# Optimization experiments

Measured on AMD Instinct MI355X. Metric: run time of the kernel, lower is better.

The kernel has to match this reference:

```python
import jax, jax.numpy as jnp
import numpy as np

N_NODES = 100000
N_EDGES = 1600000
D_IN = 128
D_OUT = 128


def setup_inputs() -> dict:
    key = jax.random.key(0)
    ks = jax.random.split(key, 8)
    x = jax.random.normal(ks[0], (N_NODES, D_IN), dtype=jnp.float32)
    edge_index = jax.random.randint(ks[1], (2, N_EDGES), 0, N_NODES, dtype=jnp.int64)
    s1 = 1.0 / np.sqrt(D_IN)
    s2 = 1.0 / np.sqrt(D_OUT)
    # SAGEConv: lin_l acts on aggregated neighbors (has bias), lin_r on self (no bias)
    Wl1 = jax.random.uniform(ks[2], (D_OUT, D_IN), jnp.float32, -s1, s1)
    Wr1 = jax.random.uniform(ks[3], (D_OUT, D_IN), jnp.float32, -s1, s1)
    b1 = jnp.zeros((D_OUT,), jnp.float32)
    Wl2 = jax.random.uniform(ks[4], (D_OUT, D_OUT), jnp.float32, -s2, s2)
    Wr2 = jax.random.uniform(ks[5], (D_OUT, D_OUT), jnp.float32, -s2, s2)
    b2 = jnp.zeros((D_OUT,), jnp.float32)
    return {"x": x, "edge_index": edge_index, "Wl1": Wl1, "Wr1": Wr1, "b1": b1,
            "Wl2": Wl2, "Wr2": Wr2, "b2": b2}


def _sage_conv(x, src, dst, Wl, Wr, b, n_nodes):
    # mean aggregation of source features at destination nodes
    agg = jax.ops.segment_sum(x[src], dst, num_segments=n_nodes)  # [N, d]
    deg = jax.ops.segment_sum(jnp.ones((src.shape[0],), x.dtype), dst, num_segments=n_nodes)
    mean = agg / jnp.maximum(deg, 1.0)[:, None]  # isolated nodes -> 0 (PyG scatter-mean)
    return mean @ Wl.T + b + x @ Wr.T


def reference(x, edge_index, Wl1, Wr1, b1, Wl2, Wr2, b2):
    src, dst = edge_index[0], edge_index[1]
    n = x.shape[0]
    h = _sage_conv(x, src, dst, Wl1, Wr1, b1, n)
    h = _sage_conv(h, src, dst, Wl2, Wr2, b2, n)
    return h
```

## Files before the change

### kernel.cpp

```cpp
#include <hip/hip_runtime.h>
#include <hip/hip_bf16.h>

#define D 128
#define SCAN_CHUNK 1024
#define TE 4096

typedef __attribute__((ext_vector_type(8))) short bf16x8;
typedef __attribute__((ext_vector_type(4))) float f32x4;
typedef __attribute__((ext_vector_type(2))) float f32x2;

__device__ __forceinline__ bool ei_is64(const int* ei32) {
    return (ei32[1] | ei32[3] | ei32[5] | ei32[7]) == 0;
}
__device__ __forceinline__ int get_idx(const void* ei, bool is64, long long pos) {
    return is64 ? (int)((const long long*)ei)[pos] : ((const int*)ei)[pos];
}

__global__ __launch_bounds__(256) void prep_kernel(
    const float* __restrict__ x, unsigned* __restrict__ xq, long long ND, int ncvt,
    const float* __restrict__ Wl1, const float* __restrict__ Wr1,
    const float* __restrict__ Wl2, const float* __restrict__ Wr2,
    ushort* __restrict__ Wf1, ushort* __restrict__ Wf2,
    const void* __restrict__ ei, int E, int NB, int NBLK, int SH,
    int* __restrict__ histT) {
    __shared__ int h[512];
    const int t = threadIdx.x;
    int bid = blockIdx.x;

    if (bid < ncvt) {
        long long i = ((long long)bid * 256 + t) * 8;
        if (i + 7 < ND) {
            float4 v0 = *reinterpret_cast<const float4*>(x + i);
            float4 v1 = *reinterpret_cast<const float4*>(x + i + 4);
            int p0 = __builtin_amdgcn_cvt_pk_fp8_f32(v0.x, v0.y, 0, false);
            p0 = __builtin_amdgcn_cvt_pk_fp8_f32(v0.z, v0.w, p0, true);
            int p1 = __builtin_amdgcn_cvt_pk_fp8_f32(v1.x, v1.y, 0, false);
            p1 = __builtin_amdgcn_cvt_pk_fp8_f32(v1.z, v1.w, p1, true);
            *reinterpret_cast<uint2*>(reinterpret_cast<unsigned char*>(xq) + i) =
                make_uint2((unsigned)p0, (unsigned)p1);
        } else {
            for (; i < ND; ++i) {
                int pk = __builtin_amdgcn_cvt_pk_fp8_f32(x[i], x[i], 0, false);
                reinterpret_cast<unsigned char*>(xq)[i] = (unsigned char)(pk & 0xff);
            }
        }
        return;
    }
    bid -= ncvt;
    if (bid < 32) {
        int gid = bid * 256 + t;
        int id = gid & 4095;
        const float* Wl = Wl1; const float* Wr = Wr1; ushort* Wf = Wf1;
        if (gid >= 4096) { Wl = Wl2; Wr = Wr2; Wf = Wf2; }
        int lane = id & 63, s = (id >> 6) & 7, j = id >> 9;
        int c = j * 16 + (lane & 15);
        int k = s * 32 + ((lane >> 4) << 3);
        const float* src = (k < 128) ? (Wl + c * 128 + k) : (Wr + c * 128 + (k - 128));
        float4 v0 = *reinterpret_cast<const float4*>(src);
        float4 v1 = *reinterpret_cast<const float4*>(src + 4);
        __hip_bfloat16 o[8];
        o[0] = __float2bfloat16(v0.x); o[1] = __float2bfloat16(v0.y);
        o[2] = __float2bfloat16(v0.z); o[3] = __float2bfloat16(v0.w);
        o[4] = __float2bfloat16(v1.x); o[5] = __float2bfloat16(v1.y);
        o[6] = __float2bfloat16(v1.z); o[7] = __float2bfloat16(v1.w);
        *reinterpret_cast<uint4*>(Wf + (size_t)id * 8) = *reinterpret_cast<uint4*>(o);
        return;
    }
    bid -= 32;
    for (int b = t; b < 512; b += 256) h[b] = 0;
    bool is64 = ei_is64((const int*)ei);
    __syncthreads();
    const int base = bid * TE;
    for (int i = t; i < TE; i += 256) {
        int e = base + i;
        if (e < E) {
            int d = get_idx(ei, is64, (long long)E + e);
            atomicAdd(&h[d >> SH], 1);
        }
    }
    __syncthreads();
    for (int b = t; b < NB; b += 256) histT[b * NBLK + bid] = h[b];
}

__global__ __launch_bounds__(256) void scan_partial_kernel(int* __restrict__ arr, int Ntot,
                                                           int* __restrict__ bsum) {
    __shared__ int ws[256];
    const int t = threadIdx.x;
    const int i0 = blockIdx.x * SCAN_CHUNK + t * 4;
    int4 v = {0, 0, 0, 0};
    if (i0 + 3 < Ntot) {
        v = *reinterpret_cast<const int4*>(arr + i0);
    } else {
        if (i0 < Ntot) v.x = arr[i0];
        if (i0 + 1 < Ntot) v.y = arr[i0 + 1];
        if (i0 + 2 < Ntot) v.z = arr[i0 + 2];
        if (i0 + 3 < Ntot) v.w = arr[i0 + 3];
    }
    ws[t] = v.x + v.y + v.z + v.w;
    __syncthreads();
    for (int off = 1; off < 256; off <<= 1) {
        int val = (t >= off) ? ws[t - off] : 0;
        __syncthreads();
        ws[t] += val;
        __syncthreads();
    }
    int ex = t ? ws[t - 1] : 0;
    int e0 = ex, e1 = ex + v.x, e2 = e1 + v.y, e3 = e2 + v.z;
    if (i0 + 3 < Ntot) {
        *reinterpret_cast<int4*>(arr + i0) = make_int4(e0, e1, e2, e3);
    } else {
        if (i0 < Ntot) arr[i0] = e0;
        if (i0 + 1 < Ntot) arr[i0 + 1] = e1;
        if (i0 + 2 < Ntot) arr[i0 + 2] = e2;
        if (i0 + 3 < Ntot) arr[i0 + 3] = e3;
    }
    if (t == 255) bsum[blockIdx.x] = ws[255];
}

__device__ __forceinline__ void scan_bsum_lds(const int* __restrict__ bsum, int nb2,
                                              int* sb) {
    const int t = threadIdx.x;
    sb[t] = (t < nb2) ? bsum[t] : 0;
    __syncthreads();
    for (int off = 1; off < 256; off <<= 1) {
        int v = (t >= off) ? sb[t - off] : 0;
        __syncthreads();
        sb[t] += v;
        __syncthreads();
    }
}

__global__ __launch_bounds__(256) void part_scatter_kernel(const void* __restrict__ ei, int E,
                                                           int NB, int NBLK, int SH,
                                                           const int* __restrict__ histT,
                                                           const int* __restrict__ bsum,
                                                           int nb2,
                                                           unsigned* __restrict__ ebuf) {
    __shared__ int cur[512];
    __shared__ int sb[256];
    const int t = threadIdx.x;
    bool is64 = ei_is64((const int*)ei);
    scan_bsum_lds(bsum, nb2, sb);
    for (int b = t; b < NB; b += 256) {
        int idx = b * NBLK + blockIdx.x;
        int c = idx >> 10;
        cur[b] = histT[idx] + (c ? sb[c - 1] : 0);
    }
    __syncthreads();
    const int base = blockIdx.x * TE;
    for (int i = t; i < TE; i += 256) {
        int e = base + i;
        if (e < E) {
            int s = get_idx(ei, is64, e);
            int d = get_idx(ei, is64, (long long)E + e);
            int pos = atomicAdd(&cur[d >> SH], 1);
            ebuf[pos] = (unsigned)s | ((unsigned)(d & ((1 << SH) - 1)) << 24);
        }
    }
}

__global__ __launch_bounds__(256) void bucket_csr_kernel(const unsigned* __restrict__ ebuf,
                                                         const int* __restrict__ histT,
                                                         const int* __restrict__ bsum,
                                                         int nb2,
                                                         int NB, int NBLK, int SH, int E,
                                                         int N, int* __restrict__ rs,
                                                         int* __restrict__ col) {
    const int b = blockIdx.x, t = threadIdx.x;
    const int nodes = 1 << SH;
    __shared__ int h[256];
    __shared__ int cur[256];
    __shared__ int sb[256];
    __shared__ int sse[2];
    scan_bsum_lds(bsum, nb2, sb);
    if (t == 0) {
        int i0 = b * NBLK;
        int c0 = i0 >> 10;
        sse[0] = histT[i0] + (c0 ? sb[c0 - 1] : 0);
        if (b + 1 < NB) {
            int i1 = (b + 1) * NBLK;
            int c1 = i1 >> 10;
            sse[1] = histT[i1] + (c1 ? sb[c1 - 1] : 0);
        } else {
            sse[1] = E;
        }
    }
    h[t] = 0;
    __syncthreads();
    const int bstart = sse[0], bend = sse[1];
    for (int i = bstart + t; i < bend; i += 256) {
        atomicAdd(&h[ebuf[i] >> 24], 1);
    }
    __syncthreads();
    for (int off = 1; off < nodes; off <<= 1) {
        int v = (t >= off) ? h[t - off] : 0;
        __syncthreads();
        h[t] += v;
        __syncthreads();
    }
    const int node0 = b << SH;
    {
        int node = node0 + t;
        if (node < N) rs[node] = bstart + h[t];
        cur[t] = bstart + (t ? h[t - 1] : 0);
    }
    __syncthreads();
    for (int i = bstart + t; i < bend; i += 256) {
        unsigned ed = ebuf[i];
        int pos = atomicAdd(&cur[ed >> 24], 1);
        col[pos] = (int)(ed & 0xFFFFFFu);
    }
}

__device__ __forceinline__ void acc8(f32x2& a0, f32x2& a1, f32x2& a2, f32x2& a3,
                                     uint2 d) {
    a0 += __builtin_amdgcn_cvt_pk_f32_fp8((int)d.x, false);
    a1 += __builtin_amdgcn_cvt_pk_f32_fp8((int)d.x, true);
    a2 += __builtin_amdgcn_cvt_pk_f32_fp8((int)d.y, false);
    a3 += __builtin_amdgcn_cvt_pk_f32_fp8((int)d.y, true);
}

__global__ __launch_bounds__(256) void aggregate_mean_fp8_kernel(
    const unsigned char* __restrict__ xq, const int* __restrict__ rs,
    const int* __restrict__ col, ushort* __restrict__ outm, int N) {
    const int t = threadIdx.x;
    const int v = blockIdx.x * 16 + (t >> 4);
    if (v >= N) return;
    const unsigned lcoff = (unsigned)(t & 15) * 8u;
    const int start = v ? rs[v - 1] : 0, end = rs[v];
    f32x2 a0 = {0.f, 0.f}, a1 = {0.f, 0.f}, a2 = {0.f, 0.f}, a3 = {0.f, 0.f};
    int e = start;
    for (; e + 7 < end; e += 8) {
        int c0 = col[e], c1 = col[e + 1], c2 = col[e + 2], c3 = col[e + 3];
        int c4 = col[e + 4], c5 = col[e + 5], c6 = col[e + 6], c7 = col[e + 7];
        uint2 d0 = *reinterpret_cast<const uint2*>(xq + (((unsigned)c0) << 7) + lcoff);
        uint2 d1 = *reinterpret_cast<const uint2*>(xq + (((unsigned)c1) << 7) + lcoff);
        uint2 d2 = *reinterpret_cast<const uint2*>(xq + (((unsigned)c2) << 7) + lcoff);
        uint2 d3 = *reinterpret_cast<const uint2*>(xq + (((unsigned)c3) << 7) + lcoff);
        uint2 d4 = *reinterpret_cast<const uint2*>(xq + (((unsigned)c4) << 7) + lcoff);
        uint2 d5 = *reinterpret_cast<const uint2*>(xq + (((unsigned)c5) << 7) + lcoff);
        uint2 d6 = *reinterpret_cast<const uint2*>(xq + (((unsigned)c6) << 7) + lcoff);
        uint2 d7 = *reinterpret_cast<const uint2*>(xq + (((unsigned)c7) << 7) + lcoff);
        acc8(a0, a1, a2, a3, d0); acc8(a0, a1, a2, a3, d1);
        acc8(a0, a1, a2, a3, d2); acc8(a0, a1, a2, a3, d3);
        acc8(a0, a1, a2, a3, d4); acc8(a0, a1, a2, a3, d5);
        acc8(a0, a1, a2, a3, d6); acc8(a0, a1, a2, a3, d7);
    }
    for (; e + 3 < end; e += 4) {
        int c0 = col[e], c1 = col[e + 1], c2 = col[e + 2], c3 = col[e + 3];
        uint2 d0 = *reinterpret_cast<const uint2*>(xq + (((unsigned)c0) << 7) + lcoff);
        uint2 d1 = *reinterpret_cast<const uint2*>(xq + (((unsigned)c1) << 7) + lcoff);
        uint2 d2 = *reinterpret_cast<const uint2*>(xq + (((unsigned)c2) << 7) + lcoff);
        uint2 d3 = *reinterpret_cast<const uint2*>(xq + (((unsigned)c3) << 7) + lcoff);
        acc8(a0, a1, a2, a3, d0); acc8(a0, a1, a2, a3, d1);
        acc8(a0, a1, a2, a3, d2); acc8(a0, a1, a2, a3, d3);
    }
    if (e < end) {
        const int l = end - 1;
        int i1 = e + 1 < end ? e + 1 : l;
        int i2 = e + 2 < end ? e + 2 : l;
        int c0 = col[e], c1 = col[i1], c2 = col[i2];
        uint2 d0 = *reinterpret_cast<const uint2*>(xq + (((unsigned)c0) << 7) + lcoff);
        uint2 d1 = *reinterpret_cast<const uint2*>(xq + (((unsigned)c1) << 7) + lcoff);
        uint2 d2 = *reinterpret_cast<const uint2*>(xq + (((unsigned)c2) << 7) + lcoff);
        d1.x = (e + 1 < end) ? d1.x : 0u; d1.y = (e + 1 < end) ? d1.y : 0u;
        d2.x = (e + 2 < end) ? d2.x : 0u; d2.y = (e + 2 < end) ? d2.y : 0u;
        acc8(a0, a1, a2, a3, d0); acc8(a0, a1, a2, a3, d1);
        acc8(a0, a1, a2, a3, d2);
    }
    float inv = (end > start) ? 1.0f / (float)(end - start) : 0.f;
    __hip_bfloat16 o[8];
    o[0] = __float2bfloat16(a0.x * inv); o[1] = __float2bfloat16(a0.y * inv);
    o[2] = __float2bfloat16(a1.x * inv); o[3] = __float2bfloat16(a1.y * inv);
    o[4] = __float2bfloat16(a2.x * inv); o[5] = __float2bfloat16(a2.y * inv);
    o[6] = __float2bfloat16(a3.x * inv); o[7] = __float2bfloat16(a3.y * inv);
    *reinterpret_cast<uint4*>(outm + (size_t)v * D + ((t & 15) << 3)) =
        *reinterpret_cast<uint4*>(o);
}

template <typename OutT, bool DUAL, bool SELFF32>
__global__ __launch_bounds__(512) void sage_mfma_kernel(
    const ushort* __restrict__ Ab, const void* __restrict__ Sb,
    const ushort* __restrict__ Wf, const float* __restrict__ bias,
    OutT* __restrict__ out, unsigned char* __restrict__ fq, int N) {
    __shared__ uint4 ldsB[4096];
    const int t = threadIdx.x;
    {
        const uint4* g = reinterpret_cast<const uint4*>(Wf);
#pragma unroll
        for (int i = 0; i < 8; ++i) ldsB[t + i * 512] = g[t + i * 512];
    }
    __syncthreads();

    const int lane = t & 63, w = t >> 6;
    const int lm = lane & 15;
    const int ksub = (lane >> 4) * 8;
    const int mbase = blockIdx.x * 128 + w * 16;

    int r0 = mbase + lm;
    if (r0 >= N) r0 = N - 1;

    f32x4 acc[8];
#pragma unroll
    for (int j = 0; j < 8; ++j) {
        float bv = bias[j * 16 + lm];
        acc[j] = {bv, bv, bv, bv};
    }

    const ushort* A0 = Ab + (size_t)r0 * D + ksub;
    const ushort* lB = reinterpret_cast<const ushort*>(ldsB) + lane * 8;

#pragma unroll
    for (int s = 0; s < 8; ++s) {
        bf16x8 a;
        if (s < 4) {
            a = *reinterpret_cast<const bf16x8*>(A0 + s * 32);
        } else if constexpr (SELFF32) {
            const float* S0 = (const float*)Sb + (size_t)r0 * D + (s - 4) * 32 + ksub;
            float4 v0 = *reinterpret_cast<const float4*>(S0);
            float4 v1 = *reinterpret_cast<const float4*>(S0 + 4);
            __hip_bfloat16 o[8];
            o[0] = __float2bfloat16(v0.x); o[1] = __float2bfloat16(v0.y);
            o[2] = __float2bfloat16(v0.z); o[3] = __float2bfloat16(v0.w);
            o[4] = __float2bfloat16(v1.x); o[5] = __float2bfloat16(v1.y);
            o[6] = __float2bfloat16(v1.z); o[7] = __float2bfloat16(v1.w);
            a = *reinterpret_cast<bf16x8*>(o);
        } else {
            const ushort* S0 = (const ushort*)Sb + (size_t)r0 * D + ksub;
            a = *reinterpret_cast<const bf16x8*>(S0 + (s - 4) * 32);
        }
#pragma unroll
        for (int j = 0; j < 8; ++j) {
            bf16x8 b = *reinterpret_cast<const bf16x8*>(lB + (j * 8 + s) * 512);
            acc[j] = __builtin_amdgcn_mfma_f32_16x16x32_bf16(a, b, acc[j], 0, 0, 0);
        }
    }

    const int rr = (lane >> 4) * 4;
#pragma unroll
    for (int r = 0; r < 4; ++r) {
        int row = mbase + rr + r;
        if (row < N) {
#pragma unroll
            for (int j = 0; j < 8; ++j) {
                float val = acc[j][r];
                if constexpr (sizeof(OutT) == 2)
                    out[(size_t)row * D + j * 16 + lm] = __float2bfloat16(val);
                else
                    out[(size_t)row * D + j * 16 + lm] = val;
                if constexpr (DUAL) {
                    int pk = __builtin_amdgcn_cvt_pk_fp8_f32(val, val, 0, false);
                    fq[(size_t)row * D + j * 16 + lm] = (unsigned char)(pk & 0xff);
                }
            }
        }
    }
}

extern "C" void kernel_launch(void* const* d_in, const int* in_sizes, int n_in,
                              void* d_out, int out_size, void* d_ws, size_t ws_size,
                              hipStream_t stream) {
    const float* x   = (const float*)d_in[0];
    const void*  ei  = d_in[1];
    const float* Wl1 = (const float*)d_in[2];
    const float* Wr1 = (const float*)d_in[3];
    const float* b1  = (const float*)d_in[4];
    const float* Wl2 = (const float*)d_in[5];
    const float* Wr2 = (const float*)d_in[6];
    const float* b2  = (const float*)d_in[7];
    float* out = (float*)d_out;

    const int N = in_sizes[0] / D;
    const int E = in_sizes[1] / 2;
    const long long ND = (long long)N * D;

    int SH = 8;
    while (((N + (1 << SH) - 1) >> SH) > 512) ++SH;
    const int NB = (N + (1 << SH) - 1) >> SH;
    const int NBLK = (E + TE - 1) / TE;
    const int Ntot = NB * NBLK;
    const int nb2 = (Ntot + SCAN_CHUNK - 1) / SCAN_CHUNK;

    ushort* meanb = (ushort*)d_ws;
    ushort* h1b   = meanb + ND;
    ushort* Wf1   = h1b + ND;
    ushort* Wf2   = Wf1 + 32768;
    int*    rs    = (int*)(Wf2 + 32768);
    int*    col   = rs + N;
    int*      histT = (int*)meanb;
    int*      bsum  = histT + Ntot;
    unsigned* ebuf  = (unsigned*)h1b;
    unsigned char* xq  = (unsigned char*)d_out;
    unsigned char* h1q = (unsigned char*)d_out + ND;

    const int ncvt = (int)((ND / 8 + 255) / 256);

    prep_kernel<<<ncvt + 32 + NBLK, 256, 0, stream>>>(
        x, (unsigned*)xq, ND, ncvt, Wl1, Wr1, Wl2, Wr2,
        Wf1, Wf2, ei, E, NB, NBLK, SH, histT);

    scan_partial_kernel<<<nb2, 256, 0, stream>>>(histT, Ntot, bsum);
    part_scatter_kernel<<<NBLK, 256, 0, stream>>>(ei, E, NB, NBLK, SH, histT, bsum, nb2, ebuf);
    bucket_csr_kernel<<<NB, 256, 0, stream>>>(ebuf, histT, bsum, nb2, NB, NBLK, SH, E, N, rs, col);

    const int agg_grid = (N + 15) / 16;
    const int gemm_grid = (N + 127) / 128;

    aggregate_mean_fp8_kernel<<<agg_grid, 256, 0, stream>>>(xq, rs, col, meanb, N);
    sage_mfma_kernel<__hip_bfloat16, true, true><<<gemm_grid, 512, 0, stream>>>(
        meanb, x, Wf1, b1, (__hip_bfloat16*)h1b, h1q, N);

    aggregate_mean_fp8_kernel<<<agg_grid, 256, 0, stream>>>(h1q, rs, col, meanb, N);
    sage_mfma_kernel<float, false, false><<<gemm_grid, 512, 0, stream>>>(
        meanb, h1b, Wf2, b2, out, nullptr, N);
}
```

Baseline: 160.9 us.

## Sort nodes by degree within aggregation blocks to balance wavefront work

The aggregation kernel now handles 32 nodes per 512-thread block. It loads each node's CSR range into shared memory and ranks the nodes by degree, so each 64-lane wavefront processes four nodes of similar degree. This is meant to cut divergence from degree imbalance inside a wavefront. The 4-edge remainder loop is replaced by one masked 7-wide tail. The cost is two block barriers, a small rank computation per block, and redundant masked loads in the tail.

```diff
diff --git a/kernel.cpp b/kernel.cpp
--- a/kernel.cpp
+++ b/kernel.cpp
@@ -220,14 +220,36 @@
     a3 += __builtin_amdgcn_cvt_pk_f32_fp8((int)d.y, true);
 }
 
-__global__ __launch_bounds__(256) void aggregate_mean_fp8_kernel(
+__global__ __launch_bounds__(512) void aggregate_mean_fp8_kernel(
     const unsigned char* __restrict__ xq, const int* __restrict__ rs,
     const int* __restrict__ col, ushort* __restrict__ outm, int N) {
-    const int t = threadIdx.x;
-    const int v = blockIdx.x * 16 + (t >> 4);
-    if (v >= N) return;
+    __shared__ int s_start[32], s_end[32], s_map[32];
+    const int t = threadIdx.x;
+    if (t < 32) {
+        int v = blockIdx.x * 32 + t;
+        int st = 0, en = 0;
+        if (v < N) { st = v ? rs[v - 1] : 0; en = rs[v]; }
+        s_start[t] = st; s_end[t] = en;
+    }
+    __syncthreads();
+    if (t < 32) {
+        int d = s_end[t] - s_start[t];
+        int r = 0;
+#pragma unroll
+        for (int j = 0; j < 32; ++j) {
+            int dj = s_end[j] - s_start[j];
+            r += (dj < d) || (dj == d && j < t);
+        }
+        s_map[r] = t;
+    }
+    __syncthreads();
+
+    const int Q = t >> 4;
+    const int li = s_map[Q];
+    const int v = blockIdx.x * 32 + li;
+    const int start = s_start[li], end = s_end[li];
     const unsigned lcoff = (unsigned)(t & 15) * 8u;
-    const int start = v ? rs[v - 1] : 0, end = rs[v];
+
     f32x2 a0 = {0.f, 0.f}, a1 = {0.f, 0.f}, a2 = {0.f, 0.f}, a3 = {0.f, 0.f};
     int e = start;
     for (; e + 7 < end; e += 8) {
@@ -246,36 +268,44 @@
         acc8(a0, a1, a2, a3, d4); acc8(a0, a1, a2, a3, d5);
         acc8(a0, a1, a2, a3, d6); acc8(a0, a1, a2, a3, d7);
     }
-    for (; e + 3 < end; e += 4) {
-        int c0 = col[e], c1 = col[e + 1], c2 = col[e + 2], c3 = col[e + 3];
+    if (e < end) {
+        const int l = end - 1;
+        int i1 = e + 1 < end ? e + 1 : l;
+        int i2 = e + 2 < end ? e + 2 : l;
+        int i3 = e + 3 < end ? e + 3 : l;
+        int i4 = e + 4 < end ? e + 4 : l;
+        int i5 = e + 5 < end ? e + 5 : l;
+        int i6 = e + 6 < end ? e + 6 : l;
+        int c0 = col[e], c1 = col[i1], c2 = col[i2], c3 = col[i3];
+        int c4 = col[i4], c5 = col[i5], c6 = col[i6];
         uint2 d0 = *reinterpret_cast<const uint2*>(xq + (((unsigned)c0) << 7) + lcoff);
         uint2 d1 = *reinterpret_cast<const uint2*>(xq + (((unsigned)c1) << 7) + lcoff);
         uint2 d2 = *reinterpret_cast<const uint2*>(xq + (((unsigned)c2) << 7) + lcoff);
         uint2 d3 = *reinterpret_cast<const uint2*>(xq + (((unsigned)c3) << 7) + lcoff);
+        uint2 d4 = *reinterpret_cast<const uint2*>(xq + (((unsigned)c4) << 7) + lcoff);
+        uint2 d5 = *reinterpret_cast<const uint2*>(xq + (((unsigned)c5) << 7) + lcoff);
+        uint2 d6 = *reinterpret_cast<const uint2*>(xq + (((unsigned)c6) << 7) + lcoff);
+        d1.x = (e + 1 < end) ? d1.x : 0u; d1.y = (e + 1 < end) ? d1.y : 0u;
+        d2.x = (e + 2 < end) ? d2.x : 0u; d2.y = (e + 2 < end) ? d2.y : 0u;
+        d3.x = (e + 3 < end) ? d3.x : 0u; d3.y = (e + 3 < end) ? d3.y : 0u;
+        d4.x = (e + 4 < end) ? d4.x : 0u; d4.y = (e + 4 < end) ? d4.y : 0u;
+        d5.x = (e + 5 < end) ? d5.x : 0u; d5.y = (e + 5 < end) ? d5.y : 0u;
+        d6.x = (e + 6 < end) ? d6.x : 0u; d6.y = (e + 6 < end) ? d6.y : 0u;
         acc8(a0, a1, a2, a3, d0); acc8(a0, a1, a2, a3, d1);
         acc8(a0, a1, a2, a3, d2); acc8(a0, a1, a2, a3, d3);
-    }
-    if (e < end) {
-        const int l = end - 1;
-        int i1 = e + 1 < end ? e + 1 : l;
-        int i2 = e + 2 < end ? e + 2 : l;
-        int c0 = col[e], c1 = col[i1], c2 = col[i2];
-        uint2 d0 = *reinterpret_cast<const uint2*>(xq + (((unsigned)c0) << 7) + lcoff);
-        uint2 d1 = *reinterpret_cast<const uint2*>(xq + (((unsigned)c1) << 7) + lcoff);
-        uint2 d2 = *reinterpret_cast<const uint2*>(xq + (((unsigned)c2) << 7) + lcoff);
-        d1.x = (e + 1 < end) ? d1.x : 0u; d1.y = (e + 1 < end) ? d1.y : 0u;
-        d2.x = (e + 2 < end) ? d2.x : 0u; d2.y = (e + 2 < end) ? d2.y : 0u;
-        acc8(a0, a1, a2, a3, d0); acc8(a0, a1, a2, a3, d1);
-        acc8(a0, a1, a2, a3, d2);
-    }
-    float inv = (end > start) ? 1.0f / (float)(end - start) : 0.f;
-    __hip_bfloat16 o[8];
-    o[0] = __float2bfloat16(a0.x * inv); o[1] = __float2bfloat16(a0.y * inv);
-    o[2] = __float2bfloat16(a1.x * inv); o[3] = __float2bfloat16(a1.y * inv);
-    o[4] = __float2bfloat16(a2.x * inv); o[5] = __float2bfloat16(a2.y * inv);
-    o[6] = __float2bfloat16(a3.x * inv); o[7] = __float2bfloat16(a3.y * inv);
-    *reinterpret_cast<uint4*>(outm + (size_t)v * D + ((t & 15) << 3)) =
-        *reinterpret_cast<uint4*>(o);
+        acc8(a0, a1, a2, a3, d4); acc8(a0, a1, a2, a3, d5);
+        acc8(a0, a1, a2, a3, d6);
+    }
+    if (v < N) {
+        float inv = (end > start) ? 1.0f / (float)(end - start) : 0.f;
+        __hip_bfloat16 o[8];
+        o[0] = __float2bfloat16(a0.x * inv); o[1] = __float2bfloat16(a0.y * inv);
+        o[2] = __float2bfloat16(a1.x * inv); o[3] = __float2bfloat16(a1.y * inv);
+        o[4] = __float2bfloat16(a2.x * inv); o[5] = __float2bfloat16(a2.y * inv);
+        o[6] = __float2bfloat16(a3.x * inv); o[7] = __float2bfloat16(a3.y * inv);
+        *reinterpret_cast<uint4*>(outm + (size_t)v * D + ((t & 15) << 3)) =
+            *reinterpret_cast<uint4*>(o);
+    }
 }
 
 template <typename OutT, bool DUAL, bool SELFF32>
@@ -403,14 +433,14 @@
     part_scatter_kernel<<<NBLK, 256, 0, stream>>>(ei, E, NB, NBLK, SH, histT, bsum, nb2, ebuf);
     bucket_csr_kernel<<<NB, 256, 0, stream>>>(ebuf, histT, bsum, nb2, NB, NBLK, SH, E, N, rs, col);
 
-    const int agg_grid = (N + 15) / 16;
+    const int agg_grid = (N + 31) / 32;
     const int gemm_grid = (N + 127) / 128;
 
-    aggregate_mean_fp8_kernel<<<agg_grid, 256, 0, stream>>>(xq, rs, col, meanb, N);
+    aggregate_mean_fp8_kernel<<<agg_grid, 512, 0, stream>>>(xq, rs, col, meanb, N);
     sage_mfma_kernel<__hip_bfloat16, true, true><<<gemm_grid, 512, 0, stream>>>(
         meanb, x, Wf1, b1, (__hip_bfloat16*)h1b, h1q, N);
 
-    aggregate_mean_fp8_kernel<<<agg_grid, 256, 0, stream>>>(h1q, rs, col, meanb, N);
+    aggregate_mean_fp8_kernel<<<agg_grid, 512, 0, stream>>>(h1q, rs, col, meanb, N);
     sage_mfma_kernel<float, false, false><<<gemm_grid, 512, 0, stream>>>(
         meanb, h1b, Wf2, b2, out, nullptr, N);
 }
```

After: 164.0 us. About the same (+1.9%).
